# Optimization experiments

Measured on AMD Instinct MI355X. Metric: run time of the kernel, lower is better.

The kernel has to match this reference:

```python
import jax, jax.numpy as jnp
import numpy as np

D_MODEL = 1024
NUM_HEADS = 16
HEAD_DIM = D_MODEL // NUM_HEADS


def setup_inputs() -> dict:
    key = jax.random.key(0)
    k_x, k_qkv, k_o = jax.random.split(key, 3)
    B, L = 2, 2048
    x = jax.random.normal(k_x, (B, L, D_MODEL), dtype=jnp.float32)
    # torch Linear weight [out, in]; y = x @ W.T. Scale ~ kaiming-uniform-ish.
    s = 1.0 / np.sqrt(D_MODEL)
    W_qkv = jax.random.uniform(k_qkv, (3 * D_MODEL, D_MODEL), dtype=jnp.float32, minval=-s, maxval=s)
    W_o = jax.random.uniform(k_o, (D_MODEL, D_MODEL), dtype=jnp.float32, minval=-s, maxval=s)
    return {"x": x, "W_qkv": W_qkv, "W_o": W_o}


def reference(x, W_qkv, W_o):
    B, L, D = x.shape
    H, dk = NUM_HEADS, HEAD_DIM
    qkv = (x @ W_qkv.T).reshape(B, L, 3, H, dk)
    q = qkv[:, :, 0].transpose(0, 2, 1, 3)  # [B,H,L,dk]
    k = qkv[:, :, 1].transpose(0, 2, 1, 3)
    v = qkv[:, :, 2].transpose(0, 2, 1, 3)
    scale = 1.0 / np.sqrt(dk).astype(np.float32)
    attn = jnp.einsum('bhqd,bhkd->bhqk', q, k) * scale  # [B,H,L,L]
    causal = jnp.tril(jnp.ones((L, L), dtype=bool))
    attn = jnp.where(causal, attn, -jnp.inf)
    attn = jax.nn.softmax(attn, axis=-1)
    y = jnp.einsum('bhqk,bhkd->bhqd', attn, v)  # [B,H,L,dk]
    y = y.transpose(0, 2, 1, 3).reshape(B, L, D)
    return y @ W_o.T
```

## Files before the change

### kernel.cpp

```cpp
#include <hip/hip_runtime.h>

typedef unsigned short u16;
typedef unsigned int   u32;

typedef __attribute__((ext_vector_type(4))) float  f32x4;
typedef __attribute__((ext_vector_type(8))) __bf16 bf16x8;

#define B_  2
#define L_  2048
#define H_  16

__device__ static inline u16 f2bf(float f) {
  u32 u = __builtin_bit_cast(u32, f);
  u32 r = u + 0x7fffu + ((u >> 16) & 1u);
  return (u16)(r >> 16);
}
__device__ static inline u32 pack2(float a, float b) {
  return (u32)f2bf(a) | ((u32)f2bf(b) << 16);
}

__device__ static inline void gload_lds16(const u16* g, u16* lds) {
  __builtin_amdgcn_global_load_lds((__attribute__((address_space(1))) void*)(g),
                                   (__attribute__((address_space(3))) void*)(lds),
                                   16, 0, 0);
}

__global__ __launch_bounds__(256) void cvt3_kernel(
    const float4* __restrict__ a, uint2* __restrict__ ao, int na,
    const float4* __restrict__ b, uint2* __restrict__ bo, int nb,
    const float4* __restrict__ c, uint2* __restrict__ co, int nc)
{
  const int step = gridDim.x * 256;
  for (int i = blockIdx.x * 256 + threadIdx.x; i < na; i += step) {
    float4 f = a[i];
    ao[i] = make_uint2(pack2(f.x, f.y), pack2(f.z, f.w));
  }
  for (int i = blockIdx.x * 256 + threadIdx.x; i < nb; i += step) {
    float4 f = b[i];
    bo[i] = make_uint2(pack2(f.x, f.y), pack2(f.z, f.w));
  }
  for (int i = blockIdx.x * 256 + threadIdx.x; i < nc; i += step) {
    float4 f = c[i];
    co[i] = make_uint2(pack2(f.x, f.y), pack2(f.z, f.w));
  }
}

template <bool OUT_F32>
__global__ __launch_bounds__(256) void gemm_bt_kernel(
    const u16* __restrict__ A, const u16* __restrict__ Bt, void* __restrict__ Cv,
    const int K, const int N)
{
  __shared__ __attribute__((aligned(16))) u16 Al[2][128 * 64];
  __shared__ __attribute__((aligned(16))) u16 Bl[2][128 * 64];

  const int tid  = threadIdx.x;
  const int w    = tid >> 6;
  const int lane = tid & 63;
  const int m0 = blockIdx.y * 128;
  const int n0 = blockIdx.x * 128;
  const int mo = (w >> 1) * 64;
  const int no = (w & 1) * 64;

  const int srow = w * 32 + (lane >> 3);
  const int scol = (((lane & 7) ^ ((lane >> 3) & 7)) * 8);

  const f32x4 zero = {0.f, 0.f, 0.f, 0.f};
  f32x4 acc[4][4];
  #pragma unroll
  for (int i = 0; i < 4; ++i)
    #pragma unroll
    for (int j = 0; j < 4; ++j) acc[i][j] = zero;

  const int frow = lane & 15;
  const int fg   = lane >> 4;

  #pragma unroll
  for (int inst = 0; inst < 4; ++inst) {
    const int r = srow + inst * 8;
    gload_lds16(A  + (size_t)(m0 + r) * K + scol, &Al[0][(w * 32 + inst * 8) * 64]);
    gload_lds16(Bt + (size_t)(n0 + r) * K + scol, &Bl[0][(w * 32 + inst * 8) * 64]);
  }

  int cur = 0;
  for (int k0 = 0; k0 < K; k0 += 64) {
    __syncthreads();
    if (k0 + 64 < K) {
      #pragma unroll
      for (int inst = 0; inst < 4; ++inst) {
        const int r = srow + inst * 8;
        gload_lds16(A  + (size_t)(m0 + r) * K + k0 + 64 + scol, &Al[cur ^ 1][(w * 32 + inst * 8) * 64]);
        gload_lds16(Bt + (size_t)(n0 + r) * K + k0 + 64 + scol, &Bl[cur ^ 1][(w * 32 + inst * 8) * 64]);
      }
    }
    #pragma unroll
    for (int ks = 0; ks < 2; ++ks) {
      const int fco = ((ks * 4 + fg) ^ (frow & 7)) * 8;
      bf16x8 af[4], bfr[4];
      #pragma unroll
      for (int i = 0; i < 4; ++i)
        af[i] = *(const bf16x8*)&Al[cur][(mo + i * 16 + frow) * 64 + fco];
      #pragma unroll
      for (int j = 0; j < 4; ++j)
        bfr[j] = *(const bf16x8*)&Bl[cur][(no + j * 16 + frow) * 64 + fco];
      #pragma unroll
      for (int i = 0; i < 4; ++i)
        #pragma unroll
        for (int j = 0; j < 4; ++j)
          acc[i][j] = __builtin_amdgcn_mfma_f32_16x16x32_bf16(af[i], bfr[j], acc[i][j], 0, 0, 0);
    }
    cur ^= 1;
  }

  const int crow0 = m0 + mo + (lane >> 4) * 4;
  const int ccol0 = n0 + no + (lane & 15);
  #pragma unroll
  for (int i = 0; i < 4; ++i)
    #pragma unroll
    for (int j = 0; j < 4; ++j)
      #pragma unroll
      for (int r = 0; r < 4; ++r) {
        const size_t idx = (size_t)(crow0 + i * 16 + r) * N + (ccol0 + j * 16);
        if (OUT_F32) ((float*)Cv)[idx] = acc[i][j][r];
        else         ((u16*)Cv)[idx]   = f2bf(acc[i][j][r]);
      }
}

__global__ __launch_bounds__(256) void attn_mfma_kernel(const u16* __restrict__ qkv,
                                                        u16* __restrict__ y)
{
  __shared__ __attribute__((aligned(16))) u16 Kt[2][64 * 64];
  __shared__ __attribute__((aligned(16))) u32 Vtd[2][64 * 40];
  __shared__ __attribute__((aligned(16))) u32 PTd[4][16 * 40];

  const int tid  = threadIdx.x;
  const int w    = tid >> 6;
  const int lane = tid & 63;
  const int fr   = lane & 15;
  const int fg   = lane >> 4;
  const int bh   = blockIdx.x;
  const int pi   = blockIdx.y;
  const int bb   = bh >> 4;
  const int hh   = bh & 15;
  const size_t rb = (size_t)bb * L_;

  const int kkp = lane & 31;
  const int dc  = 2 * w + (lane >> 5);

  const int ksr = w * 16 + (lane >> 3);
  const int ksc = (((lane & 7) ^ ((lane >> 3) & 7)) * 8);
  const int kco0 = ((fg) ^ (fr & 7)) * 8;
  const int kco1 = ((4 + fg) ^ (fr & 7)) * 8;

  const int vro = 4 * (fg ^ (fr & 3));

  const f32x4 zero = {0.f, 0.f, 0.f, 0.f};

  for (int pass = 0; pass < 2; ++pass) {
    const int qt = pass ? (31 - pi) : pi;
    const int q0 = qt * 64;
    const int qw = q0 + w * 16;

    const bf16x8 qf0 = *(const bf16x8*)(qkv + (rb + qw + fr) * 3072 + hh * 64 + fg * 8);
    const bf16x8 qf1 = *(const bf16x8*)(qkv + (rb + qw + fr) * 3072 + hh * 64 + 32 + fg * 8);

    f32x4 oacc[4];
    #pragma unroll
    for (int mt = 0; mt < 4; ++mt) oacc[mt] = zero;
    float lsum = 0.f;

    __syncthreads();
    #pragma unroll
    for (int inst = 0; inst < 2; ++inst)
      gload_lds16(qkv + (rb + ksr + inst * 8) * 3072 + 1024 + hh * 64 + ksc,
                  &Kt[0][(w * 16 + inst * 8) * 64]);
    {
      const u16* vp = qkv + (rb + 2 * kkp) * 3072 + 2048 + hh * 64 + dc * 8;
      uint4 va = *(const uint4*)vp;
      uint4 vb = *(const uint4*)(vp + 3072);
      u16 a16[8], b16[8];
      *(uint4*)a16 = va; *(uint4*)b16 = vb;
      #pragma unroll
      for (int i = 0; i < 8; ++i)
        Vtd[0][(dc * 8 + i) * 40 + (kkp ^ (4 * (i & 3)))] = (u32)a16[i] | ((u32)b16[i] << 16);
    }

    int cur = 0;
    for (int kt = 0; kt <= q0; kt += 64) {
      __syncthreads();

      const bool havenext = (kt + 64 <= q0);
      uint4 va, vb;
      if (havenext) {
        #pragma unroll
        for (int inst = 0; inst < 2; ++inst)
          gload_lds16(qkv + (rb + kt + 64 + ksr + inst * 8) * 3072 + 1024 + hh * 64 + ksc,
                      &Kt[cur ^ 1][(w * 16 + inst * 8) * 64]);
        const u16* vp = qkv + (rb + kt + 64 + 2 * kkp) * 3072 + 2048 + hh * 64 + dc * 8;
        va = *(const uint4*)vp;
        vb = *(const uint4*)(vp + 3072);
      }

      f32x4 sacc[4];
      #pragma unroll
      for (int nt = 0; nt < 4; ++nt) sacc[nt] = zero;
      #pragma unroll
      for (int nt = 0; nt < 4; ++nt) {
        bf16x8 kf0 = *(const bf16x8*)&Kt[cur][(nt * 16 + fr) * 64 + kco0];
        sacc[nt] = __builtin_amdgcn_mfma_f32_16x16x32_bf16(kf0, qf0, sacc[nt], 0, 0, 0);
        bf16x8 kf1 = *(const bf16x8*)&Kt[cur][(nt * 16 + fr) * 64 + kco1];
        sacc[nt] = __builtin_amdgcn_mfma_f32_16x16x32_bf16(kf1, qf1, sacc[nt], 0, 0, 0);
      }

      if (kt == q0) {
        #pragma unroll
        for (int nt = 0; nt < 4; ++nt) {
          float p[4];
          #pragma unroll
          for (int r = 0; r < 4; ++r) {
            p[r] = (nt * 16 + 4 * fg + r > w * 16 + fr)
                       ? 0.f : __expf(sacc[nt][r] * 0.125f);
            lsum += p[r];
          }
          *(uint2*)&PTd[w][fr * 40 + nt * 8 + 2 * fg] =
              make_uint2(pack2(p[0], p[1]), pack2(p[2], p[3]));
        }
      } else {
        #pragma unroll
        for (int nt = 0; nt < 4; ++nt) {
          float p[4];
          #pragma unroll
          for (int r = 0; r < 4; ++r) {
            p[r] = __expf(sacc[nt][r] * 0.125f);
            lsum += p[r];
          }
          *(uint2*)&PTd[w][fr * 40 + nt * 8 + 2 * fg] =
              make_uint2(pack2(p[0], p[1]), pack2(p[2], p[3]));
        }
      }

      #pragma unroll
      for (int ks = 0; ks < 2; ++ks) {
        bf16x8 pf = *(const bf16x8*)&PTd[w][fr * 40 + ks * 16 + fg * 4];
        #pragma unroll
        for (int mt = 0; mt < 4; ++mt) {
          bf16x8 vf = *(const bf16x8*)&Vtd[cur][(mt * 16 + fr) * 40 + ks * 16 + vro];
          oacc[mt] = __builtin_amdgcn_mfma_f32_16x16x32_bf16(vf, pf, oacc[mt], 0, 0, 0);
        }
      }

      if (havenext) {
        u16 a16[8], b16[8];
        *(uint4*)a16 = va; *(uint4*)b16 = vb;
        #pragma unroll
        for (int i = 0; i < 8; ++i)
          Vtd[cur ^ 1][(dc * 8 + i) * 40 + (kkp ^ (4 * (i & 3)))] = (u32)a16[i] | ((u32)b16[i] << 16);
      }
      cur ^= 1;
    }

    lsum += __shfl_xor(lsum, 16);
    lsum += __shfl_xor(lsum, 32);
    const float inv = 1.f / lsum;

    u16* yp = y + (rb + qw + fr) * 1024 + hh * 64 + 4 * fg;
    #pragma unroll
    for (int mt = 0; mt < 4; ++mt)
      *(uint2*)(yp + mt * 16) = make_uint2(pack2(oacc[mt][0] * inv, oacc[mt][1] * inv),
                                           pack2(oacc[mt][2] * inv, oacc[mt][3] * inv));
  }
}

extern "C" void kernel_launch(void* const* d_in, const int* in_sizes, int n_in,
                              void* d_out, int out_size, void* d_ws, size_t ws_size,
                              hipStream_t stream)
{
  const float* x    = (const float*)d_in[0];
  const float* Wqkv = (const float*)d_in[1];
  const float* Wo   = (const float*)d_in[2];
  float* out = (float*)d_out;

  u16* xb    = (u16*)d_ws;
  u16* Wqkvb = xb    + (size_t)4096 * 1024;
  u16* Wob   = Wqkvb + (size_t)3072 * 1024;
  u16* qkv   = Wob   + (size_t)1024 * 1024;
  u16* y     = qkv   + (size_t)4096 * 3072;

  cvt3_kernel<<<dim3(2048), dim3(256), 0, stream>>>(
      (const float4*)x,    (uint2*)xb,    4096 * 1024 / 4,
      (const float4*)Wqkv, (uint2*)Wqkvb, 3072 * 1024 / 4,
      (const float4*)Wo,   (uint2*)Wob,   1024 * 1024 / 4);

  gemm_bt_kernel<false><<<dim3(3072 / 128, 4096 / 128), dim3(256), 0, stream>>>(
      xb, Wqkvb, qkv, 1024, 3072);
  attn_mfma_kernel<<<dim3(B_ * H_, 16), dim3(256), 0, stream>>>(qkv, y);
  gemm_bt_kernel<true><<<dim3(1024 / 128, 4096 / 128), dim3(256), 0, stream>>>(
      y, Wob, out, 1024, 1024);
}
```

Baseline: 188.7 us.

## Single-buffer GEMM LDS tiles and XOR-swizzle attention V/P shared layouts

The GEMM kernel drops its double-buffered LDS prefetch and instead loads each K tile and then synchronizes before computing, halving shared memory so more blocks can be resident per CU. The attention kernel replaces the padded (stride 40) V-transpose and P buffers with unpadded stride-32 layouts using XOR swizzling to avoid bank conflicts while shrinking LDS. The GEMM change trades load/compute overlap for occupancy and adds an extra barrier per iteration, which risks exposing global load latency.

```diff
diff --git a/kernel.cpp b/kernel.cpp
--- a/kernel.cpp
+++ b/kernel.cpp
@@ -50,8 +50,8 @@
     const u16* __restrict__ A, const u16* __restrict__ Bt, void* __restrict__ Cv,
     const int K, const int N)
 {
-  __shared__ __attribute__((aligned(16))) u16 Al[2][128 * 64];
-  __shared__ __attribute__((aligned(16))) u16 Bl[2][128 * 64];
+  __shared__ __attribute__((aligned(16))) u16 Al[128 * 64];
+  __shared__ __attribute__((aligned(16))) u16 Bl[128 * 64];
 
   const int tid  = threadIdx.x;
   const int w    = tid >> 6;
@@ -74,41 +74,31 @@
   const int frow = lane & 15;
   const int fg   = lane >> 4;
 
-  #pragma unroll
-  for (int inst = 0; inst < 4; ++inst) {
-    const int r = srow + inst * 8;
-    gload_lds16(A  + (size_t)(m0 + r) * K + scol, &Al[0][(w * 32 + inst * 8) * 64]);
-    gload_lds16(Bt + (size_t)(n0 + r) * K + scol, &Bl[0][(w * 32 + inst * 8) * 64]);
-  }
-
-  int cur = 0;
   for (int k0 = 0; k0 < K; k0 += 64) {
     __syncthreads();
-    if (k0 + 64 < K) {
-      #pragma unroll
-      for (int inst = 0; inst < 4; ++inst) {
-        const int r = srow + inst * 8;
-        gload_lds16(A  + (size_t)(m0 + r) * K + k0 + 64 + scol, &Al[cur ^ 1][(w * 32 + inst * 8) * 64]);
-        gload_lds16(Bt + (size_t)(n0 + r) * K + k0 + 64 + scol, &Bl[cur ^ 1][(w * 32 + inst * 8) * 64]);
-      }
-    }
+    #pragma unroll
+    for (int inst = 0; inst < 4; ++inst) {
+      const int r = srow + inst * 8;
+      gload_lds16(A  + (size_t)(m0 + r) * K + k0 + scol, &Al[(w * 32 + inst * 8) * 64]);
+      gload_lds16(Bt + (size_t)(n0 + r) * K + k0 + scol, &Bl[(w * 32 + inst * 8) * 64]);
+    }
+    __syncthreads();
     #pragma unroll
     for (int ks = 0; ks < 2; ++ks) {
       const int fco = ((ks * 4 + fg) ^ (frow & 7)) * 8;
       bf16x8 af[4], bfr[4];
       #pragma unroll
       for (int i = 0; i < 4; ++i)
-        af[i] = *(const bf16x8*)&Al[cur][(mo + i * 16 + frow) * 64 + fco];
+        af[i] = *(const bf16x8*)&Al[(mo + i * 16 + frow) * 64 + fco];
       #pragma unroll
       for (int j = 0; j < 4; ++j)
-        bfr[j] = *(const bf16x8*)&Bl[cur][(no + j * 16 + frow) * 64 + fco];
+        bfr[j] = *(const bf16x8*)&Bl[(no + j * 16 + frow) * 64 + fco];
       #pragma unroll
       for (int i = 0; i < 4; ++i)
         #pragma unroll
         for (int j = 0; j < 4; ++j)
           acc[i][j] = __builtin_amdgcn_mfma_f32_16x16x32_bf16(af[i], bfr[j], acc[i][j], 0, 0, 0);
     }
-    cur ^= 1;
   }
 
   const int crow0 = m0 + mo + (lane >> 4) * 4;
@@ -129,8 +119,8 @@
                                                         u16* __restrict__ y)
 {
   __shared__ __attribute__((aligned(16))) u16 Kt[2][64 * 64];
-  __shared__ __attribute__((aligned(16))) u32 Vtd[2][64 * 40];
-  __shared__ __attribute__((aligned(16))) u32 PTd[4][16 * 40];
+  __shared__ __attribute__((aligned(16))) u32 Vtd[2][64 * 32];
+  __shared__ __attribute__((aligned(16))) u32 PTd[4][16 * 32];
 
   const int tid  = threadIdx.x;
   const int w    = tid >> 6;
@@ -151,7 +141,9 @@
   const int kco0 = ((fg) ^ (fr & 7)) * 8;
   const int kco1 = ((4 + fg) ^ (fr & 7)) * 8;
 
-  const int vro = 4 * (fg ^ (fr & 3));
+  const int cro0 = 4 * ((fg) ^ (fr & 7));
+  const int cro1 = 4 * ((4 + fg) ^ (fr & 7));
+  const int pwo = 4 * (fr & 7);
 
   const f32x4 zero = {0.f, 0.f, 0.f, 0.f};
 
@@ -181,7 +173,8 @@
       *(uint4*)a16 = va; *(uint4*)b16 = vb;
       #pragma unroll
       for (int i = 0; i < 8; ++i)
-        Vtd[0][(dc * 8 + i) * 40 + (kkp ^ (4 * (i & 3)))] = (u32)a16[i] | ((u32)b16[i] << 16);
+        Vtd[0][(dc * 8 + i) * 32 + 4 * ((kkp >> 2) ^ i) + (kkp & 3)] =
+            (u32)a16[i] | ((u32)b16[i] << 16);
     }
 
     int cur = 0;
@@ -221,7 +214,7 @@
                        ? 0.f : __expf(sacc[nt][r] * 0.125f);
             lsum += p[r];
           }
-          *(uint2*)&PTd[w][fr * 40 + nt * 8 + 2 * fg] =
+          *(uint2*)&PTd[w][fr * 32 + ((8 * nt + 2 * fg) ^ pwo)] =
               make_uint2(pack2(p[0], p[1]), pack2(p[2], p[3]));
         }
       } else {
@@ -233,17 +226,17 @@
             p[r] = __expf(sacc[nt][r] * 0.125f);
             lsum += p[r];
           }
-          *(uint2*)&PTd[w][fr * 40 + nt * 8 + 2 * fg] =
+          *(uint2*)&PTd[w][fr * 32 + ((8 * nt + 2 * fg) ^ pwo)] =
               make_uint2(pack2(p[0], p[1]), pack2(p[2], p[3]));
         }
       }
 
       #pragma unroll
       for (int ks = 0; ks < 2; ++ks) {
-        bf16x8 pf = *(const bf16x8*)&PTd[w][fr * 40 + ks * 16 + fg * 4];
+        bf16x8 pf = *(const bf16x8*)&PTd[w][fr * 32 + (ks ? cro1 : cro0)];
         #pragma unroll
         for (int mt = 0; mt < 4; ++mt) {
-          bf16x8 vf = *(const bf16x8*)&Vtd[cur][(mt * 16 + fr) * 40 + ks * 16 + vro];
+          bf16x8 vf = *(const bf16x8*)&Vtd[cur][(mt * 16 + fr) * 32 + (ks ? cro1 : cro0)];
           oacc[mt] = __builtin_amdgcn_mfma_f32_16x16x32_bf16(vf, pf, oacc[mt], 0, 0, 0);
         }
       }
@@ -253,7 +246,8 @@
         *(uint4*)a16 = va; *(uint4*)b16 = vb;
         #pragma unroll
         for (int i = 0; i < 8; ++i)
-          Vtd[cur ^ 1][(dc * 8 + i) * 40 + (kkp ^ (4 * (i & 3)))] = (u32)a16[i] | ((u32)b16[i] << 16);
+          Vtd[cur ^ 1][(dc * 8 + i) * 32 + 4 * ((kkp >> 2) ^ i) + (kkp & 3)] =
+              (u32)a16[i] | ((u32)b16[i] << 16);
       }
       cur ^= 1;
     }
```

After: 184.8 us. 1.02x faster.
